# Optimization experiments

Hardware: AMD Instinct MI355X
Metric: run time of the kernel (lower is better)

The kernel has to match this reference:

```python
import jax, jax.numpy as jnp
import numpy as np


def _local_linear(x, W, b=None):
    # Faithful to Local_Linear: split last dim into G groups, apply per-group
    # Linear, then stack groups on the LAST axis and flatten -> output channel
    # index is o*G + g (interleaved), NOT block-diagonal order.
    B, N, C = x.shape
    G, og, ig = W.shape
    y = jnp.einsum('bngi,goi->bngo', x.reshape(B, N, G, ig), W)  # [B,N,G,og]
    if b is not None:
        y = y + b
    return jnp.swapaxes(y, -1, -2).reshape(B, N, G * og)  # [B,N,og,G] -> flat


def setup_inputs() -> dict:
    key = jax.random.key(0)
    ks = jax.random.split(key, 6)
    B, N, dim, H = 16, 8192, 128, 2
    hd = dim // H
    s = 1.0 / np.sqrt(hd).astype(np.float32)
    return {
        'x': jax.random.normal(ks[0], (B, N, dim), jnp.float32),
        'Wk': jax.random.normal(ks[1], (H, hd, hd), jnp.float32) * s,
        'Wv': jax.random.normal(ks[2], (H, hd, hd), jnp.float32) * s,
        'Wp': jax.random.normal(ks[3], (H, hd, hd), jnp.float32) * s,
        'bp': jax.random.normal(ks[4], (H, hd), jnp.float32) * 0.01,
        'mem': jax.random.normal(ks[5], (H, hd), jnp.float32) * 0.02,
    }


def reference(x, Wk, Wv, Wp, bp, mem):
    B, N, C = x.shape
    H, hd = mem.shape
    scale = hd ** -0.5
    # k, v: [B, H, N, hd] (view of interleaved grouped-linear output, as in torch)
    k = _local_linear(x, Wk).reshape(B, N, H, hd).transpose(0, 2, 1, 3)
    v = _local_linear(x, Wv).reshape(B, N, H, hd).transpose(0, 2, 1, 3)
    # The query (memory_bank) is identical for every position, so the [N,N]
    # attention matrix has identical rows -> compute one row per (b,h).
    s = jnp.einsum('hd,bhmd->bhm', mem, k) * scale          # logits over keys
    a = jax.nn.softmax(s, axis=-1)                          # [B,H,N]
    row = jnp.einsum('bhm,bhmd->bhd', a, v)                 # [B,H,hd]
    # torch does out.view(B,N,-1) WITHOUT permuting heads back; [B,H,N,hd]
    # reshaped directly to [B,N,C]. Replicate that exact layout.
    out = jnp.broadcast_to(row[:, :, None, :], (B, H, N, hd)).reshape(B, N, C)
    return _local_linear(out, Wp, bp)
```

## Files before the change

kernel.cpp:

```cpp
#include <hip/hip_runtime.h>
#include <hip/hip_bf16.h>

#define B_      16
#define N_      8192
#define C_      128
#define HD_     64
#define TILE_N  128
#define NBLK    (N_ / TILE_N)
#define PART_STRIDE 260

__global__ __launch_bounds__(TILE_N) void k_partial(
    const float* __restrict__ x,
    const float* __restrict__ Wk,
    const float* __restrict__ mem,
    float* __restrict__ part)
{
    __shared__ float qeff[2][C_];
    __shared__ float sl[2][TILE_N];
    __shared__ float red[2][TILE_N];

    const int t   = threadIdx.x;
    const int blk = blockIdx.x;
    const int b   = blk / NBLK;
    const int n0  = (blk % NBLK) * TILE_N;

    {
        const int c = t, g = c >> 6, i = c & 63;
        float a0 = 0.f, a1 = 0.f;
        for (int j = 0; j < 32; ++j) {
            a0 += mem[2 * j + g]      * Wk[g * 4096 + j        * 64 + i];
            a1 += mem[64 + 2 * j + g] * Wk[g * 4096 + (32 + j) * 64 + i];
        }
        qeff[0][c] = 0.125f * a0;
        qeff[1][c] = 0.125f * a1;
    }
    __syncthreads();

    const int n = n0 + t;
    const float4* xr = (const float4*)(x + ((size_t)b * N_ + n) * C_);
    float s0 = 0.f, s1 = 0.f;
    #pragma unroll
    for (int v = 0; v < 32; ++v) {
        const float4 q = xr[v];
        const int c0 = v * 4;
        s0 += q.x * qeff[0][c0]     + q.y * qeff[0][c0 + 1]
            + q.z * qeff[0][c0 + 2] + q.w * qeff[0][c0 + 3];
        s1 += q.x * qeff[1][c0]     + q.y * qeff[1][c0 + 1]
            + q.z * qeff[1][c0 + 2] + q.w * qeff[1][c0 + 3];
    }

    red[0][t] = s0; red[1][t] = s1;
    __syncthreads();
    for (int off = TILE_N / 2; off > 0; off >>= 1) {
        if (t < off) {
            red[0][t] = fmaxf(red[0][t], red[0][t + off]);
            red[1][t] = fmaxf(red[1][t], red[1][t + off]);
        }
        __syncthreads();
    }
    const float m0 = red[0][0], m1 = red[1][0];
    __syncthreads();

    const float w0 = __expf(s0 - m0), w1 = __expf(s1 - m1);
    sl[0][t] = w0; sl[1][t] = w1;
    red[0][t] = w0; red[1][t] = w1;
    __syncthreads();
    for (int off = TILE_N / 2; off > 0; off >>= 1) {
        if (t < off) {
            red[0][t] += red[0][t + off];
            red[1][t] += red[1][t + off];
        }
        __syncthreads();
    }
    const float l0 = red[0][0], l1 = red[1][0];

    const int c = t;
    const float* xcol = x + ((size_t)b * N_ + n0) * C_ + c;
    float a0 = 0.f, a1 = 0.f;
    for (int r = 0; r < TILE_N; ++r) {
        const float xf = xcol[(size_t)r * C_];
        a0 += sl[0][r] * xf;
        a1 += sl[1][r] * xf;
    }

    float* p = part + (size_t)blk * PART_STRIDE;
    p[4 + c]       = a0;
    p[4 + 128 + c] = a1;
    if (t == 0) { p[0] = m0; p[1] = m1; p[2] = l0; p[3] = l1; }
}

__global__ __launch_bounds__(256) void k_combine(
    const float* __restrict__ part,
    const float* __restrict__ Wv,
    const float* __restrict__ Wp,
    const float* __restrict__ bp,
    float* __restrict__ Fbuf)
{
    __shared__ float ml[4][NBLK];
    __shared__ float xan[2][C_];
    __shared__ float rowv[2][HD_];

    const int t = threadIdx.x;
    const int b = blockIdx.x;

    if (t < NBLK) {
        const float* p = part + ((size_t)b * NBLK + t) * PART_STRIDE;
        ml[0][t] = p[0]; ml[1][t] = p[1]; ml[2][t] = p[2]; ml[3][t] = p[3];
    }
    __syncthreads();

    const int h = t >> 7, c = t & 127;
    float M = -1e30f;
    for (int k = 0; k < NBLK; ++k) M = fmaxf(M, ml[h][k]);
    float L = 0.f;
    for (int k = 0; k < NBLK; ++k) L += ml[2 + h][k] * __expf(ml[h][k] - M);
    float xa = 0.f;
    for (int k = 0; k < NBLK; ++k) {
        const float* p = part + ((size_t)b * NBLK + k) * PART_STRIDE;
        xa += p[4 + h * C_ + c] * __expf(ml[h][k] - M);
    }
    xan[h][c] = xa / L;
    __syncthreads();

    if (t < 128) {
        const int hh = t >> 6, d = t & 63, g = d & 1, o = hh * 32 + (d >> 1);
        const float* wv = Wv + g * 4096 + o * 64;
        const float* xv = &xan[hh][g * 64];
        float acc = 0.f;
        for (int i = 0; i < 64; ++i) acc += xv[i] * wv[i];
        rowv[hh][d] = acc;
    }
    __syncthreads();

    {
        const int hh = t >> 7, cc = t & 127, g = cc & 1, o = cc >> 1;
        const float* wp = Wp + g * 4096 + o * 64;
        float acc = bp[g * 64 + o];
        for (int i = 0; i < 64; ++i) acc += rowv[hh][i] * wp[i];
        Fbuf[(b * 2 + hh) * C_ + cc] = acc;
    }
}

__global__ __launch_bounds__(256) void k_bcast(
    const float4* __restrict__ F4,
    float4* __restrict__ out4)
{
    __shared__ float4 Ftab[1024];
    const int t = threadIdx.x;
    for (int i = t; i < 1024; i += 256) Ftab[i] = F4[i];
    __syncthreads();

    size_t idx = (size_t)blockIdx.x * 256 + t;
    const size_t stride = (size_t)2048 * 256;
    #pragma unroll
    for (int k = 0; k < 8; ++k) {
        out4[idx] = Ftab[((idx >> 17) << 5) | (idx & 31)];
        idx += stride;
    }
}

extern "C" void kernel_launch(void* const* d_in, const int* in_sizes, int n_in,
                              void* d_out, int out_size, void* d_ws, size_t ws_size,
                              hipStream_t stream)
{
    const float* x   = (const float*)d_in[0];
    const float* Wk  = (const float*)d_in[1];
    const float* Wv  = (const float*)d_in[2];
    const float* Wp  = (const float*)d_in[3];
    const float* bp  = (const float*)d_in[4];
    const float* mem = (const float*)d_in[5];

    float* part = (float*)d_ws;
    float* Fbuf = (float*)((char*)d_ws + (size_t)B_ * NBLK * PART_STRIDE * sizeof(float));

    k_partial<<<dim3(B_ * NBLK), dim3(TILE_N), 0, stream>>>(x, Wk, mem, part);
    k_combine<<<dim3(B_), dim3(256), 0, stream>>>(part, Wv, Wp, bp, Fbuf);
    k_bcast<<<dim3(2048), dim3(256), 0, stream>>>((const float4*)Fbuf,
                                                  (float4*)d_out);
}
```

Measured before the change: 149.7 us.

## Double threads in partial kernel, use wave shuffles, nontemporal broadcast stores

The partial kernel now runs 256 threads per tile. Each half computes part of the logit dot products and half of the weighted x accumulation, and the halves are combined through shared memory. The tree reductions that needed many block barriers become wavefront shuffle reductions plus one cross-wave step. The broadcast kernel writes output with nontemporal stores so the 64MB output stream does not pollute the cache. The aim is more parallelism per tile and fewer synchronisations, at the cost of extra shared-memory combine steps.

After: 144.1 us. 1.04x faster.

```diff
diff --git a/kernel.cpp b/kernel.cpp
--- a/kernel.cpp
+++ b/kernel.cpp
@@ -9,15 +9,19 @@
 #define NBLK    (N_ / TILE_N)
 #define PART_STRIDE 260
 
-__global__ __launch_bounds__(TILE_N) void k_partial(
+typedef float v4f __attribute__((ext_vector_type(4)));
+
+__global__ __launch_bounds__(256) void k_partial(
     const float* __restrict__ x,
     const float* __restrict__ Wk,
     const float* __restrict__ mem,
     float* __restrict__ part)
 {
-    __shared__ float qeff[2][C_];
-    __shared__ float sl[2][TILE_N];
-    __shared__ float red[2][TILE_N];
+    __shared__ float qeff0[C_], qeff1[C_];
+    __shared__ float sp0[2][TILE_N], sp1[2][TILE_N];
+    __shared__ float sl0[TILE_N], sl1[TILE_N];
+    __shared__ float pa0[2][C_], pa1[2][C_];
+    __shared__ float redm[8];
 
     const int t   = threadIdx.x;
     const int blk = blockIdx.x;
@@ -25,68 +29,95 @@
     const int n0  = (blk % NBLK) * TILE_N;
 
     {
-        const int c = t, g = c >> 6, i = c & 63;
+        const int h = t >> 7, c = t & 127, g = c >> 6, i = c & 63;
+        const float* wkb = Wk + g * 4096 + (h * 32) * 64 + i;
+        const float* mr  = mem + h * 64 + g;
+        float a = 0.f;
+        #pragma unroll
+        for (int j = 0; j < 32; ++j) a += mr[2 * j] * wkb[j * 64];
+        if (h == 0) qeff0[c] = 0.125f * a; else qeff1[c] = 0.125f * a;
+    }
+    __syncthreads();
+
+    const int r = t & 127, half = t >> 7;
+    {
+        const float4* xr = (const float4*)(x + ((size_t)b * N_ + n0 + r) * C_ + half * 64);
+        float p0 = 0.f, p1 = 0.f;
+        #pragma unroll
+        for (int v = 0; v < 16; ++v) {
+            const float4 q = xr[v];
+            const int c0 = half * 64 + v * 4;
+            p0 += q.x * qeff0[c0]     + q.y * qeff0[c0 + 1]
+                + q.z * qeff0[c0 + 2] + q.w * qeff0[c0 + 3];
+            p1 += q.x * qeff1[c0]     + q.y * qeff1[c0 + 1]
+                + q.z * qeff1[c0 + 2] + q.w * qeff1[c0 + 3];
+        }
+        sp0[half][r] = p0;
+        sp1[half][r] = p1;
+    }
+    __syncthreads();
+
+    float s0 = 0.f, s1 = 0.f;
+    if (t < TILE_N) {
+        s0 = sp0[0][t] + sp0[1][t];
+        s1 = sp1[0][t] + sp1[1][t];
+    }
+    float m0 = s0, m1 = s1;
+    #pragma unroll
+    for (int off = 32; off > 0; off >>= 1) {
+        m0 = fmaxf(m0, __shfl_xor(m0, off));
+        m1 = fmaxf(m1, __shfl_xor(m1, off));
+    }
+    if (t == 0)  { redm[0] = m0; redm[1] = m1; }
+    if (t == 64) { redm[2] = m0; redm[3] = m1; }
+    __syncthreads();
+    m0 = fmaxf(redm[0], redm[2]);
+    m1 = fmaxf(redm[1], redm[3]);
+
+    float w0 = 0.f, w1 = 0.f;
+    if (t < TILE_N) {
+        w0 = __expf(s0 - m0);
+        w1 = __expf(s1 - m1);
+        sl0[t] = w0;
+        sl1[t] = w1;
+    }
+    float l0 = w0, l1 = w1;
+    #pragma unroll
+    for (int off = 32; off > 0; off >>= 1) {
+        l0 += __shfl_xor(l0, off);
+        l1 += __shfl_xor(l1, off);
+    }
+    if (t == 0)  { redm[4] = l0; redm[5] = l1; }
+    if (t == 64) { redm[6] = l0; redm[7] = l1; }
+    __syncthreads();
+
+    {
+        const int c = t & 127, rh = t >> 7;
+        const float* xcol = x + ((size_t)b * N_ + n0 + rh * 64) * C_ + c;
+        const float* wr0 = &sl0[rh * 64];
+        const float* wr1 = &sl1[rh * 64];
         float a0 = 0.f, a1 = 0.f;
-        for (int j = 0; j < 32; ++j) {
-            a0 += mem[2 * j + g]      * Wk[g * 4096 + j        * 64 + i];
-            a1 += mem[64 + 2 * j + g] * Wk[g * 4096 + (32 + j) * 64 + i];
+        #pragma unroll 8
+        for (int k = 0; k < 64; ++k) {
+            const float xf = xcol[(size_t)k * C_];
+            a0 += wr0[k] * xf;
+            a1 += wr1[k] * xf;
         }
-        qeff[0][c] = 0.125f * a0;
-        qeff[1][c] = 0.125f * a1;
-    }
-    __syncthreads();
-
-    const int n = n0 + t;
-    const float4* xr = (const float4*)(x + ((size_t)b * N_ + n) * C_);
-    float s0 = 0.f, s1 = 0.f;
-    #pragma unroll
-    for (int v = 0; v < 32; ++v) {
-        const float4 q = xr[v];
-        const int c0 = v * 4;
-        s0 += q.x * qeff[0][c0]     + q.y * qeff[0][c0 + 1]
-            + q.z * qeff[0][c0 + 2] + q.w * qeff[0][c0 + 3];
-        s1 += q.x * qeff[1][c0]     + q.y * qeff[1][c0 + 1]
-            + q.z * qeff[1][c0 + 2] + q.w * qeff[1][c0 + 3];
-    }
-
-    red[0][t] = s0; red[1][t] = s1;
-    __syncthreads();
-    for (int off = TILE_N / 2; off > 0; off >>= 1) {
-        if (t < off) {
-            red[0][t] = fmaxf(red[0][t], red[0][t + off]);
-            red[1][t] = fmaxf(red[1][t], red[1][t + off]);
-        }
-        __syncthreads();
-    }
-    const float m0 = red[0][0], m1 = red[1][0];
-    __syncthreads();
-
-    const float w0 = __expf(s0 - m0), w1 = __expf(s1 - m1);
-    sl[0][t] = w0; sl[1][t] = w1;
-    red[0][t] = w0; red[1][t] = w1;
-    __syncthreads();
-    for (int off = TILE_N / 2; off > 0; off >>= 1) {
-        if (t < off) {
-            red[0][t] += red[0][t + off];
-            red[1][t] += red[1][t + off];
-        }
-        __syncthreads();
-    }
-    const float l0 = red[0][0], l1 = red[1][0];
-
-    const int c = t;
-    const float* xcol = x + ((size_t)b * N_ + n0) * C_ + c;
-    float a0 = 0.f, a1 = 0.f;
-    for (int r = 0; r < TILE_N; ++r) {
-        const float xf = xcol[(size_t)r * C_];
-        a0 += sl[0][r] * xf;
-        a1 += sl[1][r] * xf;
-    }
+        pa0[rh][c] = a0;
+        pa1[rh][c] = a1;
+    }
+    __syncthreads();
 
     float* p = part + (size_t)blk * PART_STRIDE;
-    p[4 + c]       = a0;
-    p[4 + 128 + c] = a1;
-    if (t == 0) { p[0] = m0; p[1] = m1; p[2] = l0; p[3] = l1; }
+    if (t < C_) {
+        p[4 + t]       = pa0[0][t] + pa0[1][t];
+        p[4 + C_ + t]  = pa1[0][t] + pa1[1][t];
+    }
+    if (t == 0) {
+        p[0] = m0; p[1] = m1;
+        p[2] = redm[4] + redm[6];
+        p[3] = redm[5] + redm[7];
+    }
 }
 
 __global__ __launch_bounds__(256) void k_combine(
@@ -142,10 +173,10 @@
 }
 
 __global__ __launch_bounds__(256) void k_bcast(
-    const float4* __restrict__ F4,
-    float4* __restrict__ out4)
-{
-    __shared__ float4 Ftab[1024];
+    const v4f* __restrict__ F4,
+    v4f* __restrict__ out4)
+{
+    __shared__ v4f Ftab[1024];
     const int t = threadIdx.x;
     for (int i = t; i < 1024; i += 256) Ftab[i] = F4[i];
     __syncthreads();
@@ -154,7 +185,8 @@
     const size_t stride = (size_t)2048 * 256;
     #pragma unroll
     for (int k = 0; k < 8; ++k) {
-        out4[idx] = Ftab[((idx >> 17) << 5) | (idx & 31)];
+        const v4f v = Ftab[((idx >> 17) << 5) | (idx & 31)];
+        __builtin_nontemporal_store(v, &out4[idx]);
         idx += stride;
     }
 }
@@ -173,8 +205,8 @@
     float* part = (float*)d_ws;
     float* Fbuf = (float*)((char*)d_ws + (size_t)B_ * NBLK * PART_STRIDE * sizeof(float));
 
-    k_partial<<<dim3(B_ * NBLK), dim3(TILE_N), 0, stream>>>(x, Wk, mem, part);
+    k_partial<<<dim3(B_ * NBLK), dim3(256), 0, stream>>>(x, Wk, mem, part);
     k_combine<<<dim3(B_), dim3(256), 0, stream>>>(part, Wv, Wp, bp, Fbuf);
-    k_bcast<<<dim3(2048), dim3(256), 0, stream>>>((const float4*)Fbuf,
-                                                  (float4*)d_out);
-}
+    k_bcast<<<dim3(2048), dim3(256), 0, stream>>>((const v4f*)Fbuf,
+                                                  (v4f*)d_out);
+}
```
